# Performance work log

Hardware: AMD Instinct MI355X
Metric: run time of the kernel (lower is better)

Reference implementation:

```python
import jax, jax.numpy as jnp
import numpy as np

PAD, SOS, EOS = 0, 1, 2
NEG = -10000.0


def _lstm(x, w_ih, w_hh, b, reverse):
    # x: [T,B,E]; torch gate order i,f,g,o; b = b_ih + b_hh combined
    T, B, _ = x.shape
    H = w_hh.shape[1]
    xg = jnp.einsum('tbe,ge->tbg', x, w_ih) + b  # precompute input gates [T,B,4H]

    def step(carry, g):
        h, c = carry
        g = g + h @ w_hh.T
        i, f, gg, o = jnp.split(g, 4, axis=-1)
        c = jax.nn.sigmoid(f) * c + jax.nn.sigmoid(i) * jnp.tanh(gg)
        h = jax.nn.sigmoid(o) * jnp.tanh(c)
        return (h, c), h

    init = (jnp.zeros((B, H), x.dtype), jnp.zeros((B, H), x.dtype))
    _, hs = jax.lax.scan(step, init, xg, reverse=reverse)
    return hs  # [T,B,H]


def setup_inputs() -> dict:
    key = jax.random.key(0)
    T, B, V, E, H, K = 256, 64, 50000, 512, 512, 24
    ks = jax.random.split(key, 12)
    xw = jax.random.randint(ks[0], (T, B), 4, V)
    y_tags = jax.random.randint(ks[1], (T, B), 3, K)  # real tags, > EOS so mask is all ones
    y0 = jnp.concatenate([jnp.full((1, B), SOS, dtype=y_tags.dtype), y_tags], axis=0)  # [T+1,B]
    s = lambda k, sh: (jax.random.normal(k, sh, jnp.float32) * 0.02)
    emb = s(ks[2], (V, E))
    w_ih_f = s(ks[3], (4 * H, E)); w_hh_f = s(ks[4], (4 * H, H)); b_f = jnp.zeros((4 * H,), jnp.float32)
    w_ih_b = s(ks[5], (4 * H, E)); w_hh_b = s(ks[6], (4 * H, H)); b_b = jnp.zeros((4 * H,), jnp.float32)
    w_out = s(ks[7], (K, 2 * H)); b_out = jnp.zeros((K,), jnp.float32)
    trans = jax.random.normal(ks[8], (K, K), jnp.float32)
    trans = trans.at[SOS, :].set(NEG).at[:, EOS].set(NEG).at[:, PAD].set(NEG).at[PAD, :].set(NEG)
    trans = trans.at[PAD, EOS].set(0.0).at[PAD, PAD].set(0.0)
    return dict(xw=xw, y0=y0, emb=emb, w_ih_f=w_ih_f, w_hh_f=w_hh_f, b_f=b_f,
                w_ih_b=w_ih_b, w_hh_b=w_hh_b, b_b=b_b, w_out=w_out, b_out=b_out, trans=trans)


def reference(xw, y0, emb, w_ih_f, w_hh_f, b_f, w_ih_b, w_hh_b, b_b, w_out, b_out, trans):
    mask = (y0[1:] > PAD).astype(emb.dtype)  # [T,B]
    x = emb[xw]  # [T,B,E]
    hf = _lstm(x, w_ih_f, w_hh_f, b_f, reverse=False)
    hb = _lstm(x, w_ih_b, w_hh_b, b_b, reverse=True)
    h = jnp.concatenate([hf, hb], axis=-1) @ w_out.T + b_out  # [T,B,K]
    h = h * mask[:, :, None]
    B, K = h.shape[1], h.shape[2]

    # --- CRF partition function (forward algorithm) ---
    score0 = jnp.full((B, K), NEG, h.dtype).at[:, SOS].set(0.0)

    def step(score, inp):
        ht, mt = inp  # ht: [B,K], mt: [B]
        # new[b,j] = logsumexp_i(score[b,i] + ht[b,j] + trans[j,i])
        new = jax.nn.logsumexp(score[:, None, :] + ht[:, :, None] + trans[None, :, :], axis=2)
        return new * mt[:, None] + score * (1.0 - mt[:, None]), None

    score, _ = jax.lax.scan(step, score0, (h, mask))
    Z = jax.nn.logsumexp(score + trans[EOS], axis=1)  # [B]

    # --- gold path score ---
    emit = jnp.take_along_axis(h, y0[1:][:, :, None], axis=2)[..., 0]  # [T,B]
    tr = trans[y0[1:], y0[:-1]]  # [T,B]
    lens = mask.sum(0).astype(jnp.int32)  # [B]
    last = jnp.take_along_axis(y0, lens[None, :], axis=0)[0]  # y0[lens[b], b]
    gold = ((emit + tr) * mask).sum(0) + trans[EOS, last]  # [B]

    return jnp.mean(Z - gold)
```

## Files before the change

kernel.cpp:

```cpp
#include <hip/hip_runtime.h>

typedef __attribute__((ext_vector_type(8))) short short8;
typedef __attribute__((ext_vector_type(4))) float f32x4;

#define NEGV -10000.0f

__device__ __forceinline__ float bfu2f(unsigned short u) {
  unsigned int x = ((unsigned int)u) << 16;
  return __builtin_bit_cast(float, x);
}
__device__ __forceinline__ unsigned short f2bfu(float f) {
  unsigned int x = __builtin_bit_cast(unsigned int, f);
  x += 0x7fffu + ((x >> 16) & 1u);
  return (unsigned short)(x >> 16);
}
__device__ __forceinline__ float fsig(float x) {
  return 1.0f / (1.0f + __expf(-x));
}
__device__ __forceinline__ float ftanh(float x) {
  x = fminf(15.0f, fmaxf(-15.0f, x));
  float e = __expf(-2.0f * x);
  return (1.0f - e) / (1.0f + e);
}

__global__ __launch_bounds__(256) void prep_kernel(
    const float* __restrict__ wihf, const float* __restrict__ wihb,
    const float* __restrict__ whhf, const float* __restrict__ whhb,
    const float* __restrict__ wo, const float* __restrict__ bfv,
    const float* __restrict__ bbv,
    unsigned short* __restrict__ wih_c, unsigned short* __restrict__ whh_c,
    unsigned short* __restrict__ wout_c, float* __restrict__ bias_c) {
  size_t i = (size_t)blockIdx.x * 256 + threadIdx.x;
  const size_t n_half = 2048u * 512u;
  const size_t n_wih = 2u * n_half;
  const size_t n_wo = 24u * 1024u;
  if (i < n_wih) {
    float v = (i < n_half) ? wihf[i] : wihb[i - n_half];
    wih_c[i] = f2bfu(v);
  } else if (i < 2u * n_wih) {
    size_t j = i - n_wih;
    float v = (j < n_half) ? whhf[j] : whhb[j - n_half];
    whh_c[j] = f2bfu(v);
  } else if (i < 2u * n_wih + n_wo) {
    size_t j = i - 2u * n_wih;
    wout_c[j] = f2bfu(wo[j]);
  } else if (i < 2u * n_wih + n_wo + 4096u) {
    size_t j = i - 2u * n_wih - n_wo;
    bias_c[j] = (j < 2048u) ? bfv[j] : bbv[j - 2048u];
  }
}

__global__ __launch_bounds__(64) void gather_kernel(
    const int* __restrict__ xw, const float* __restrict__ emb,
    unsigned short* __restrict__ xbf) {
  int tb = blockIdx.x;
  int l = threadIdx.x;
  int tok = xw[tb];
  const float* src = emb + (size_t)tok * 512 + l * 8;
  short8 o;
#pragma unroll
  for (int j = 0; j < 8; ++j) o[j] = (short)f2bfu(src[j]);
  *(short8*)(xbf + (size_t)tb * 512 + l * 8) = o;
}

__global__ __launch_bounds__(256) void gemm_xg_kernel(
    const unsigned short* __restrict__ A,
    const unsigned short* __restrict__ Bm,
    const float* __restrict__ bias,
    unsigned short* __restrict__ C) {
  __shared__ alignas(16) char As[16384];
  __shared__ alignas(16) char Bs[16384];
  int m0 = blockIdx.x * 128, n0 = blockIdx.y * 128;
  int tid = threadIdx.x;
  int wv = tid >> 6, l = tid & 63;
  int wm = wv >> 1, wn = wv & 1;
  int col = l & 15, quad = l >> 4;
  f32x4 zero4 = {0.f, 0.f, 0.f, 0.f};
  f32x4 acc[4][4];
#pragma unroll
  for (int i = 0; i < 4; ++i)
#pragma unroll
    for (int j = 0; j < 4; ++j) acc[i][j] = zero4;
  for (int kt = 0; kt < 8; ++kt) {
#pragma unroll
    for (int q = 0; q < 4; ++q) {
      int o = q * 4096 + tid * 16;
      int row = o >> 7;
      int cb = o & 127;
      int swz = cb ^ ((row & 7) << 4);
      short8 va = *(const short8*)(A + (size_t)(m0 + row) * 512 + kt * 64 + (cb >> 1));
      *(short8*)(As + row * 128 + swz) = va;
      short8 vb = *(const short8*)(Bm + (size_t)(n0 + row) * 512 + kt * 64 + (cb >> 1));
      *(short8*)(Bs + row * 128 + swz) = vb;
    }
    __syncthreads();
#pragma unroll
    for (int kk = 0; kk < 2; ++kk) {
      short8 af[4], bf8[4];
#pragma unroll
      for (int mi = 0; mi < 4; ++mi) {
        int r = wm * 64 + mi * 16 + col;
        int cb = kk * 64 + quad * 16;
        af[mi] = *(const short8*)(As + r * 128 + (cb ^ ((r & 7) << 4)));
      }
#pragma unroll
      for (int ni = 0; ni < 4; ++ni) {
        int r = wn * 64 + ni * 16 + col;
        int cb = kk * 64 + quad * 16;
        bf8[ni] = *(const short8*)(Bs + r * 128 + (cb ^ ((r & 7) << 4)));
      }
#pragma unroll
      for (int mi = 0; mi < 4; ++mi)
#pragma unroll
        for (int ni = 0; ni < 4; ++ni)
          acc[mi][ni] = __builtin_amdgcn_mfma_f32_16x16x32_bf16(af[mi], bf8[ni], acc[mi][ni], 0, 0, 0);
    }
    __syncthreads();
  }
#pragma unroll
  for (int ni = 0; ni < 4; ++ni) {
    int cg = n0 + wn * 64 + ni * 16 + col;
    float bv = bias[cg];
#pragma unroll
    for (int mi = 0; mi < 4; ++mi) {
#pragma unroll
      for (int r = 0; r < 4; ++r) {
        int rg = m0 + wm * 64 + mi * 16 + quad * 4 + r;
        C[(size_t)rg * 4096 + cg] = f2bfu(acc[mi][ni][r] + bv);
      }
    }
  }
}

__global__ __launch_bounds__(64, 1) void scan_kernel(
    const unsigned short* __restrict__ whh,
    const unsigned short* __restrict__ xg,
    unsigned short* __restrict__ hfp,
    unsigned short* __restrict__ hbp) {
  __shared__ alignas(16) unsigned short tbuf[128];
  int wid = blockIdx.x;
  int l = threadIdx.x;
  int dir = wid & 1;
  int g = (wid >> 1) & 63;
  int wv = (wid >> 7) & 3;
  int u0 = g * 8;
  int col = l & 15, quad = l >> 4;
  int b_row = wv * 16 + quad * 4;
  short8 bfr[2][16];
#pragma unroll
  for (int n = 0; n < 2; ++n) {
    int blk = n * 2 + (col >> 3);
    int gr = blk * 512 + u0 + (col & 7);
    const char* base = (const char*)(whh + ((size_t)dir * 2048 + gr) * 512 + quad * 8);
#pragma unroll
    for (int kk = 0; kk < 16; ++kk)
      asm volatile("global_load_dwordx4 %0, %1, off" : "=v"(bfr[n][kk]) : "v"(base + kk * 64));
  }
  asm volatile("s_waitcnt vmcnt(0)" ::: "memory");
  unsigned short* hseq = dir ? hbp : hfp;
  float cst[4] = {0.f, 0.f, 0.f, 0.f};
  f32x4 zero4 = {0.f, 0.f, 0.f, 0.f};
  for (int s = 0; s < 256; ++s) {
    int t = dir ? (255 - s) : s;
    float xgv[2][4];
#pragma unroll
    for (int n = 0; n < 2; ++n) {
      int gc = dir * 2048 + (n * 2 + (col >> 3)) * 512 + u0 + (col & 7);
#pragma unroll
      for (int r = 0; r < 4; ++r)
        xgv[n][r] = bfu2f(xg[((size_t)t * 64 + b_row + r) * 4096 + gc]);
    }
    f32x4 a0 = zero4, a1 = zero4;
    if (s > 0) {
      int tprev = dir ? (t + 1) : (t - 1);
      const char* pbase = (const char*)hseq + (size_t)tprev * 65536 + quad * 1024 +
                          (wv * 16 + col) * 16;
      short8 af[16];
      unsigned long long bal;
      do {
#pragma unroll
        for (int kk = 0; kk < 16; ++kk)
          asm volatile("global_load_dwordx4 %0, %1, off sc0 sc1" : "=v"(af[kk]) : "v"(pbase + kk * 4096));
        asm volatile("s_waitcnt vmcnt(0)" ::: "memory");
        unsigned int anystale = 0u;
#pragma unroll
        for (int kk = 0; kk < 16; ++kk)
          anystale |= (((unsigned short)af[kk][0]) == 0xFFFFu) ? 1u : 0u;
        bal = __ballot(anystale != 0u);
      } while (bal != 0ull);
      __builtin_amdgcn_sched_barrier(0);
#pragma unroll
      for (int kk = 0; kk < 16; ++kk) {
        a0 = __builtin_amdgcn_mfma_f32_16x16x32_bf16(af[kk], bfr[0][kk], a0, 0, 0, 0);
        a1 = __builtin_amdgcn_mfma_f32_16x16x32_bf16(af[kk], bfr[1][kk], a1, 0, 0, 0);
      }
    }
    {
      bool low = (col < 8);
#pragma unroll
      for (int r = 0; r < 4; ++r) {
        float g0 = a0[r] + xgv[0][r];
        float g1 = a1[r] + xgv[1][r];
        float p0 = __shfl_xor(g0, 8);
        float p1 = __shfl_xor(g1, 8);
        float iv = low ? g0 : p0;
        float fv = low ? p0 : g0;
        float gv = low ? g1 : p1;
        float ov = low ? p1 : g1;
        float cn = fsig(fv) * cst[r] + fsig(iv) * ftanh(gv);
        cst[r] = cn;
        float hv = fsig(ov) * ftanh(cn);
        if (low) tbuf[(quad * 4 + r) * 8 + (col & 7)] = f2bfu(hv);
      }
    }
    asm volatile("s_waitcnt lgkmcnt(0)" ::: "memory");
    if (l < 16) {
      short8 hrow = *(const short8*)(tbuf + l * 8);
      char* dst = (char*)hseq + (size_t)t * 65536 + g * 1024 + (wv * 16 + l) * 16;
      asm volatile("global_store_dwordx4 %0, %1, off sc0 sc1" :: "v"(dst), "v"(hrow) : "memory");
    }
  }
}

__global__ __launch_bounds__(256) void logits_kernel(
    const unsigned short* __restrict__ hfp, const unsigned short* __restrict__ hbp,
    const unsigned short* __restrict__ wout, const float* __restrict__ bout,
    const int* __restrict__ y0, float* __restrict__ lg) {
  int t = blockIdx.x, tid = threadIdx.x;
  int b = tid >> 2, ks = tid & 3;
  int ytag = y0[(t + 1) * 64 + b];
  float mk = (ytag > 0) ? 1.f : 0.f;
  float av[6] = {0.f, 0.f, 0.f, 0.f, 0.f, 0.f};
  const char* pf = (const char*)hfp + (size_t)t * 65536;
  const char* pb = (const char*)hbp + (size_t)t * 65536;
  for (int uc = 0; uc < 64; ++uc) {
    short8 hv = *(const short8*)(pf + uc * 1024 + b * 16);
#pragma unroll
    for (int kk = 0; kk < 6; ++kk) {
      int k = ks * 6 + kk;
      short8 wv = *(const short8*)(wout + (size_t)k * 1024 + uc * 8);
#pragma unroll
      for (int j = 0; j < 8; ++j)
        av[kk] += bfu2f((unsigned short)hv[j]) * bfu2f((unsigned short)wv[j]);
    }
  }
  for (int uc = 0; uc < 64; ++uc) {
    short8 hv = *(const short8*)(pb + uc * 1024 + b * 16);
#pragma unroll
    for (int kk = 0; kk < 6; ++kk) {
      int k = ks * 6 + kk;
      short8 wv = *(const short8*)(wout + (size_t)k * 1024 + 512 + uc * 8);
#pragma unroll
      for (int j = 0; j < 8; ++j)
        av[kk] += bfu2f((unsigned short)hv[j]) * bfu2f((unsigned short)wv[j]);
    }
  }
#pragma unroll
  for (int kk = 0; kk < 6; ++kk) {
    int k = ks * 6 + kk;
    lg[((size_t)t * 64 + b) * 32 + k] = mk * (av[kk] + bout[k]);
  }
}

__global__ __launch_bounds__(64) void crf_kernel(
    const float* __restrict__ lg, const int* __restrict__ y0,
    const float* __restrict__ trans, float* __restrict__ res) {
  int b = blockIdx.x, l = threadIdx.x;
  __shared__ float tl[600];
  __shared__ float sc[24];
  for (int i = l; i < 576; i += 64) tl[(i / 24) * 25 + (i % 24)] = trans[i];
  if (l < 24) sc[l] = (l == 1) ? 0.f : NEGV;
  __syncthreads();
  float gold = 0.f;
  int lens = 0;
  for (int t = l; t < 256; t += 64) {
    int y1 = y0[(t + 1) * 64 + b];
    int yp = y0[t * 64 + b];
    if (y1 > 0) {
      gold += lg[((size_t)t * 64 + b) * 32 + y1] + tl[y1 * 25 + yp];
      lens += 1;
    }
  }
#pragma unroll
  for (int off = 32; off > 0; off >>= 1) {
    gold += __shfl_down(gold, off);
    lens += __shfl_down(lens, off);
  }
  gold = __shfl(gold, 0);
  lens = __shfl(lens, 0);
  int last = y0[lens * 64 + b];
  gold += tl[2 * 25 + last];
  int lc = (l < 24) ? l : 23;
  float trow[24];
#pragma unroll
  for (int j = 0; j < 24; ++j) trow[j] = tl[lc * 25 + j];
  for (int t = 0; t < 256; ++t) {
    int y1 = y0[(t + 1) * 64 + b];
    if (y1 > 0) {
      float ns = 0.f;
      if (l < 24) {
        float ht = lg[((size_t)t * 64 + b) * 32 + l];
        float mx = -3.0e38f;
        float sj[24];
#pragma unroll
        for (int j = 0; j < 24; ++j) {
          sj[j] = sc[j] + trow[j];
          mx = fmaxf(mx, sj[j]);
        }
        float sm = 0.f;
#pragma unroll
        for (int j = 0; j < 24; ++j) sm += __expf(sj[j] - mx);
        ns = ht + mx + __logf(sm);
      }
      __syncthreads();
      if (l < 24) sc[l] = ns;
      __syncthreads();
    }
  }
  float v = (l < 24) ? sc[l] + tl[2 * 25 + l] : -3.0e38f;
  float mx = v;
#pragma unroll
  for (int off = 32; off > 0; off >>= 1) mx = fmaxf(mx, __shfl_xor(mx, off));
  float se = (l < 24) ? __expf(v - mx) : 0.f;
#pragma unroll
  for (int off = 32; off > 0; off >>= 1) se += __shfl_xor(se, off);
  float Z = mx + __logf(se);
  if (l == 0) res[b] = Z - gold;
}

__global__ __launch_bounds__(64) void reduce_kernel(const float* __restrict__ res,
                                                    float* __restrict__ out) {
  int l = threadIdx.x;
  float v = res[l];
#pragma unroll
  for (int off = 32; off > 0; off >>= 1) v += __shfl_down(v, off);
  if (l == 0) out[0] = v * (1.0f / 64.0f);
}

extern "C" void kernel_launch(void* const* d_in, const int* in_sizes, int n_in,
                              void* d_out, int out_size, void* d_ws, size_t ws_size,
                              hipStream_t stream) {
  (void)in_sizes; (void)n_in; (void)out_size; (void)ws_size;
  const int* xw = (const int*)d_in[0];
  const int* y0 = (const int*)d_in[1];
  const float* emb = (const float*)d_in[2];
  const float* wihf = (const float*)d_in[3];
  const float* whhf = (const float*)d_in[4];
  const float* bfv = (const float*)d_in[5];
  const float* wihb = (const float*)d_in[6];
  const float* whhb = (const float*)d_in[7];
  const float* bbv = (const float*)d_in[8];
  const float* wo = (const float*)d_in[9];
  const float* bo = (const float*)d_in[10];
  const float* tr = (const float*)d_in[11];
  char* ws = (char*)d_ws;
  unsigned short* xg = (unsigned short*)(ws + 0);
  unsigned short* xbf = (unsigned short*)(ws + 134217728);
  unsigned short* wih_c = (unsigned short*)(ws + 150994944);
  unsigned short* whh_c = (unsigned short*)(ws + 155189248);
  unsigned short* wout_c = (unsigned short*)(ws + 159383552);
  float* bias_c = (float*)(ws + 159432704);
  unsigned short* hfp = (unsigned short*)(ws + 159449088);
  unsigned short* hbp = (unsigned short*)(ws + 176226304);
  float* lg = (float*)(ws + 193003520);
  float* res = (float*)(ws + 195104768);

  hipMemsetAsync(hfp, 0xFF, 16777216, stream);
  hipMemsetAsync(hbp, 0xFF, 16777216, stream);
  prep_kernel<<<16496, 256, 0, stream>>>(wihf, wihb, whhf, whhb, wo, bfv, bbv,
                                         wih_c, whh_c, wout_c, bias_c);
  gather_kernel<<<16384, 64, 0, stream>>>(xw, emb, xbf);
  gemm_xg_kernel<<<dim3(128, 32), 256, 0, stream>>>(xbf, wih_c, bias_c, xg);
  scan_kernel<<<512, 64, 0, stream>>>(whh_c, xg, hfp, hbp);
  logits_kernel<<<256, 256, 0, stream>>>(hfp, hbp, wout_c, bo, y0, lg);
  crf_kernel<<<64, 64, 0, stream>>>(lg, y0, tr, res);
  reduce_kernel<<<1, 64, 0, stream>>>(res, (float*)d_out);
}
```

Baseline: 1.250 ms.

## Speed up LSTM scan polling with L2-scoped loads, xg prefetch, and block remap

```diff
diff --git a/kernel.cpp b/kernel.cpp
--- a/kernel.cpp
+++ b/kernel.cpp
@@ -140,9 +140,10 @@
   __shared__ alignas(16) unsigned short tbuf[128];
   int wid = blockIdx.x;
   int l = threadIdx.x;
-  int dir = wid & 1;
-  int g = (wid >> 1) & 63;
-  int wv = (wid >> 7) & 3;
+  int c = wid & 7;
+  int dir = c & 1;
+  int wv = (c >> 1) & 3;
+  int g = wid >> 3;
   int u0 = g * 8;
   int col = l & 15, quad = l >> 4;
   int b_row = wv * 16 + quad * 4;
@@ -156,70 +157,110 @@
     for (int kk = 0; kk < 16; ++kk)
       asm volatile("global_load_dwordx4 %0, %1, off" : "=v"(bfr[n][kk]) : "v"(base + kk * 64));
   }
-  asm volatile("s_waitcnt vmcnt(0)" ::: "memory");
   unsigned short* hseq = dir ? hbp : hfp;
+  int gc0 = dir * 2048 + (col >> 3) * 512 + u0 + (col & 7);
   float cst[4] = {0.f, 0.f, 0.f, 0.f};
   f32x4 zero4 = {0.f, 0.f, 0.f, 0.f};
-  for (int s = 0; s < 256; ++s) {
-    int t = dir ? (255 - s) : s;
-    float xgv[2][4];
-#pragma unroll
-    for (int n = 0; n < 2; ++n) {
-      int gc = dir * 2048 + (n * 2 + (col >> 3)) * 512 + u0 + (col & 7);
-#pragma unroll
-      for (int r = 0; r < 4; ++r)
-        xgv[n][r] = bfu2f(xg[((size_t)t * 64 + b_row + r) * 4096 + gc]);
-    }
-    f32x4 a0 = zero4, a1 = zero4;
-    if (s > 0) {
-      int tprev = dir ? (t + 1) : (t - 1);
-      const char* pbase = (const char*)hseq + (size_t)tprev * 65536 + quad * 1024 +
-                          (wv * 16 + col) * 16;
-      short8 af[16];
-      unsigned long long bal;
-      do {
-#pragma unroll
-        for (int kk = 0; kk < 16; ++kk)
-          asm volatile("global_load_dwordx4 %0, %1, off sc0 sc1" : "=v"(af[kk]) : "v"(pbase + kk * 4096));
-        asm volatile("s_waitcnt vmcnt(0)" ::: "memory");
-        unsigned int anystale = 0u;
-#pragma unroll
-        for (int kk = 0; kk < 16; ++kk)
-          anystale |= (((unsigned short)af[kk][0]) == 0xFFFFu) ? 1u : 0u;
-        bal = __ballot(anystale != 0u);
-      } while (bal != 0ull);
-      __builtin_amdgcn_sched_barrier(0);
-#pragma unroll
-      for (int kk = 0; kk < 16; ++kk) {
-        a0 = __builtin_amdgcn_mfma_f32_16x16x32_bf16(af[kk], bfr[0][kk], a0, 0, 0, 0);
-        a1 = __builtin_amdgcn_mfma_f32_16x16x32_bf16(af[kk], bfr[1][kk], a1, 0, 0, 0);
-      }
-    }
-    {
-      bool low = (col < 8);
-#pragma unroll
-      for (int r = 0; r < 4; ++r) {
-        float g0 = a0[r] + xgv[0][r];
-        float g1 = a1[r] + xgv[1][r];
-        float p0 = __shfl_xor(g0, 8);
-        float p1 = __shfl_xor(g1, 8);
-        float iv = low ? g0 : p0;
-        float fv = low ? p0 : g0;
-        float gv = low ? g1 : p1;
-        float ov = low ? p1 : g1;
-        float cn = fsig(fv) * cst[r] + fsig(iv) * ftanh(gv);
-        cst[r] = cn;
-        float hv = fsig(ov) * ftanh(cn);
-        if (low) tbuf[(quad * 4 + r) * 8 + (col & 7)] = f2bfu(hv);
-      }
-    }
-    asm volatile("s_waitcnt lgkmcnt(0)" ::: "memory");
-    if (l < 16) {
-      short8 hrow = *(const short8*)(tbuf + l * 8);
-      char* dst = (char*)hseq + (size_t)t * 65536 + g * 1024 + (wv * 16 + l) * 16;
-      asm volatile("global_store_dwordx4 %0, %1, off sc0 sc1" :: "v"(dst), "v"(hrow) : "memory");
-    }
-  }
+  short8 af[16];
+  int usefast = 1;
+  unsigned int xA[8], xB[8];
+  {
+    int t0 = dir ? 255 : 0;
+#pragma unroll
+    for (int r = 0; r < 4; ++r) {
+      const char* xa = (const char*)(xg + ((size_t)t0 * 64 + b_row + r) * 4096 + gc0);
+      asm volatile("global_load_ushort %0, %1, off" : "=v"(xA[r]) : "v"(xa));
+      asm volatile("global_load_ushort %0, %1, off" : "=v"(xA[4 + r]) : "v"(xa + 2048));
+    }
+  }
+  asm volatile("s_waitcnt vmcnt(0)" ::: "memory");
+  __builtin_amdgcn_sched_barrier(0);
+
+#define SCAN_STEP(S_, XU_, XP_)                                                             \
+  {                                                                                         \
+    int s_ = (S_);                                                                          \
+    int t_ = dir ? (255 - s_) : s_;                                                         \
+    f32x4 a0 = zero4, a1 = zero4;                                                           \
+    if (s_ > 0) {                                                                           \
+      int tprev = t_ + (dir ? 1 : -1);                                                      \
+      const char* pbase = (const char*)hseq + (size_t)tprev * 65536 + quad * 1024 +         \
+                          (wv * 16 + col) * 16;                                             \
+      unsigned long long bal = 1ull;                                                        \
+      if (usefast) {                                                                        \
+        for (int tryi = 0; tryi < 8 && bal != 0ull; ++tryi) {                               \
+          _Pragma("unroll") for (int kk = 0; kk < 16; ++kk)                                 \
+              asm volatile("global_load_dwordx4 %0, %1, off sc0"                            \
+                           : "=v"(af[kk]) : "v"(pbase + kk * 4096));                        \
+          asm volatile("s_waitcnt vmcnt(0)" ::: "memory");                                  \
+          __builtin_amdgcn_sched_barrier(0);                                                \
+          unsigned int st_ = 0u;                                                            \
+          _Pragma("unroll") for (int kk = 0; kk < 16; ++kk)                                 \
+              st_ |= (((unsigned short)af[kk][0]) == 0xFFFFu) ? 1u : 0u;                    \
+          bal = __ballot(st_ != 0u);                                                        \
+        }                                                                                   \
+        if (bal != 0ull) usefast = 0;                                                       \
+      }                                                                                     \
+      while (bal != 0ull) {                                                                 \
+        _Pragma("unroll") for (int kk = 0; kk < 16; ++kk)                                   \
+            asm volatile("global_load_dwordx4 %0, %1, off sc0 sc1"                          \
+                         : "=v"(af[kk]) : "v"(pbase + kk * 4096));                          \
+        asm volatile("s_waitcnt vmcnt(0)" ::: "memory");                                    \
+        __builtin_amdgcn_sched_barrier(0);                                                  \
+        unsigned int st_ = 0u;                                                              \
+        _Pragma("unroll") for (int kk = 0; kk < 16; ++kk)                                   \
+            st_ |= (((unsigned short)af[kk][0]) == 0xFFFFu) ? 1u : 0u;                      \
+        bal = __ballot(st_ != 0u);                                                          \
+      }                                                                                     \
+      __builtin_amdgcn_s_setprio(1);                                                        \
+      __builtin_amdgcn_sched_barrier(0);                                                    \
+      _Pragma("unroll") for (int kk = 0; kk < 16; ++kk) {                                   \
+        a0 = __builtin_amdgcn_mfma_f32_16x16x32_bf16(af[kk], bfr[0][kk], a0, 0, 0, 0);      \
+        a1 = __builtin_amdgcn_mfma_f32_16x16x32_bf16(af[kk], bfr[1][kk], a1, 0, 0, 0);      \
+      }                                                                                     \
+    }                                                                                       \
+    {                                                                                       \
+      int sn = (s_ < 255) ? (s_ + 1) : 255;                                                 \
+      int tn = dir ? (255 - sn) : sn;                                                       \
+      _Pragma("unroll") for (int r = 0; r < 4; ++r) {                                       \
+        const char* xa = (const char*)(xg + ((size_t)tn * 64 + b_row + r) * 4096 + gc0);    \
+        asm volatile("global_load_ushort %0, %1, off" : "=v"(XP_[r]) : "v"(xa));            \
+        asm volatile("global_load_ushort %0, %1, off" : "=v"(XP_[4 + r]) : "v"(xa + 2048)); \
+      }                                                                                     \
+    }                                                                                       \
+    {                                                                                       \
+      bool low = (col < 8);                                                                 \
+      _Pragma("unroll") for (int r = 0; r < 4; ++r) {                                       \
+        float g0 = a0[r] + bfu2f((unsigned short)XU_[r]);                                   \
+        float g1 = a1[r] + bfu2f((unsigned short)XU_[4 + r]);                               \
+        float p0 = __shfl_xor(g0, 8);                                                       \
+        float p1 = __shfl_xor(g1, 8);                                                       \
+        float iv = low ? g0 : p0;                                                           \
+        float fv = low ? p0 : g0;                                                           \
+        float gv = low ? g1 : p1;                                                           \
+        float ov = low ? p1 : g1;                                                           \
+        float cn = fsig(fv) * cst[r] + fsig(iv) * ftanh(gv);                                \
+        cst[r] = cn;                                                                        \
+        float hv = fsig(ov) * ftanh(cn);                                                    \
+        if (low) tbuf[(quad * 4 + r) * 8 + (col & 7)] = f2bfu(hv);                          \
+      }                                                                                     \
+    }                                                                                       \
+    asm volatile("s_waitcnt lgkmcnt(0)" ::: "memory");                                      \
+    if (l < 16) {                                                                           \
+      short8 hrow = *(const short8*)(tbuf + l * 8);                                         \
+      char* dst = (char*)hseq + (size_t)t_ * 65536 + g * 1024 + (wv * 16 + l) * 16;         \
+      asm volatile("global_store_dwordx4 %0, %1, off sc0 sc1" ::"v"(dst), "v"(hrow)         \
+                   : "memory");                                                             \
+      asm volatile("global_store_dwordx4 %0, %1, off sc0" ::"v"(dst), "v"(hrow)             \
+                   : "memory");                                                             \
+    }                                                                                       \
+    __builtin_amdgcn_s_setprio(0);                                                          \
+  }
+
+  for (int it = 0; it < 128; ++it) {
+    SCAN_STEP(2 * it, xA, xB);
+    SCAN_STEP(2 * it + 1, xB, xA);
+  }
+#undef SCAN_STEP
 }
 
 __global__ __launch_bounds__(256) void logits_kernel(
```

After: 1.208 ms. 1.04x faster.

## Fuse embedding gather, input-gate GEMM and LSTM scan into one persistent kernel

Applied to the files above, without the earlier changes.

```diff
diff --git a/kernel.cpp b/kernel.cpp
--- a/kernel.cpp
+++ b/kernel.cpp
@@ -50,174 +50,203 @@
   }
 }
 
-__global__ __launch_bounds__(64) void gather_kernel(
-    const int* __restrict__ xw, const float* __restrict__ emb,
-    unsigned short* __restrict__ xbf) {
-  int tb = blockIdx.x;
-  int l = threadIdx.x;
-  int tok = xw[tb];
-  const float* src = emb + (size_t)tok * 512 + l * 8;
-  short8 o;
-#pragma unroll
-  for (int j = 0; j < 8; ++j) o[j] = (short)f2bfu(src[j]);
-  *(short8*)(xbf + (size_t)tb * 512 + l * 8) = o;
-}
-
-__global__ __launch_bounds__(256) void gemm_xg_kernel(
-    const unsigned short* __restrict__ A,
-    const unsigned short* __restrict__ Bm,
+__global__ __launch_bounds__(256, 1) void fused_kernel(
+    const int* __restrict__ xw,
+    const float* __restrict__ emb,
+    const unsigned short* __restrict__ wih,
     const float* __restrict__ bias,
-    unsigned short* __restrict__ C) {
+    const unsigned short* __restrict__ whh,
+    unsigned short* __restrict__ xg,
+    unsigned short* __restrict__ hfp,
+    unsigned short* __restrict__ hbp) {
   __shared__ alignas(16) char As[16384];
   __shared__ alignas(16) char Bs[16384];
-  int m0 = blockIdx.x * 128, n0 = blockIdx.y * 128;
-  int tid = threadIdx.x;
-  int wv = tid >> 6, l = tid & 63;
-  int wm = wv >> 1, wn = wv & 1;
-  int col = l & 15, quad = l >> 4;
-  f32x4 zero4 = {0.f, 0.f, 0.f, 0.f};
-  f32x4 acc[4][4];
-#pragma unroll
-  for (int i = 0; i < 4; ++i)
-#pragma unroll
-    for (int j = 0; j < 4; ++j) acc[i][j] = zero4;
-  for (int kt = 0; kt < 8; ++kt) {
-#pragma unroll
-    for (int q = 0; q < 4; ++q) {
-      int o = q * 4096 + tid * 16;
-      int row = o >> 7;
-      int cb = o & 127;
-      int swz = cb ^ ((row & 7) << 4);
-      short8 va = *(const short8*)(A + (size_t)(m0 + row) * 512 + kt * 64 + (cb >> 1));
-      *(short8*)(As + row * 128 + swz) = va;
-      short8 vb = *(const short8*)(Bm + (size_t)(n0 + row) * 512 + kt * 64 + (cb >> 1));
-      *(short8*)(Bs + row * 128 + swz) = vb;
-    }
-    __syncthreads();
-#pragma unroll
-    for (int kk = 0; kk < 2; ++kk) {
-      short8 af[4], bf8[4];
+  int gid = blockIdx.x;
+  if (gid < 4096) {
+    int bx = gid >> 5, by = gid & 31;
+    int m_eff = (bx & 1) ? (127 - (bx >> 1)) : (bx >> 1);
+    int m0 = m_eff * 128, n0 = by * 128;
+    int tid = threadIdx.x;
+    int wv = tid >> 6, l = tid & 63;
+    int wm = wv >> 1, wn = wv & 1;
+    int col = l & 15, quad = l >> 4;
+    int tok[4];
+#pragma unroll
+    for (int q = 0; q < 4; ++q) tok[q] = xw[m0 + ((q * 4096 + tid * 16) >> 7)];
+    f32x4 zero4 = {0.f, 0.f, 0.f, 0.f};
+    f32x4 acc[4][4];
+#pragma unroll
+    for (int i = 0; i < 4; ++i)
+#pragma unroll
+      for (int j = 0; j < 4; ++j) acc[i][j] = zero4;
+    for (int kt = 0; kt < 8; ++kt) {
+#pragma unroll
+      for (int q = 0; q < 4; ++q) {
+        int o = q * 4096 + tid * 16;
+        int row = o >> 7;
+        int cb = o & 127;
+        int swz = cb ^ ((row & 7) << 4);
+        const float* sa = emb + (size_t)tok[q] * 512 + kt * 64 + (cb >> 1);
+        f32x4 f0 = *(const f32x4*)sa;
+        f32x4 f1 = *(const f32x4*)(sa + 4);
+        short8 va;
+#pragma unroll
+        for (int j = 0; j < 4; ++j) {
+          va[j] = (short)f2bfu(f0[j]);
+          va[4 + j] = (short)f2bfu(f1[j]);
+        }
+        *(short8*)(As + row * 128 + swz) = va;
+        short8 vb = *(const short8*)(wih + (size_t)(n0 + row) * 512 + kt * 64 + (cb >> 1));
+        *(short8*)(Bs + row * 128 + swz) = vb;
+      }
+      __syncthreads();
+#pragma unroll
+      for (int kk = 0; kk < 2; ++kk) {
+        short8 af[4], bf8[4];
+#pragma unroll
+        for (int mi = 0; mi < 4; ++mi) {
+          int r = wm * 64 + mi * 16 + col;
+          int cb = kk * 64 + quad * 16;
+          af[mi] = *(const short8*)(As + r * 128 + (cb ^ ((r & 7) << 4)));
+        }
+#pragma unroll
+        for (int ni = 0; ni < 4; ++ni) {
+          int r = wn * 64 + ni * 16 + col;
+          int cb = kk * 64 + quad * 16;
+          bf8[ni] = *(const short8*)(Bs + r * 128 + (cb ^ ((r & 7) << 4)));
+        }
+#pragma unroll
+        for (int mi = 0; mi < 4; ++mi)
+#pragma unroll
+          for (int ni = 0; ni < 4; ++ni)
+            acc[mi][ni] = __builtin_amdgcn_mfma_f32_16x16x32_bf16(af[mi], bf8[ni], acc[mi][ni], 0, 0, 0);
+      }
+      __syncthreads();
+    }
+#pragma unroll
+    for (int ni = 0; ni < 4; ++ni) {
+      int cg = n0 + wn * 64 + ni * 16 + col;
+      float bv = bias[cg];
 #pragma unroll
       for (int mi = 0; mi < 4; ++mi) {
-        int r = wm * 64 + mi * 16 + col;
-        int cb = kk * 64 + quad * 16;
-        af[mi] = *(const short8*)(As + r * 128 + (cb ^ ((r & 7) << 4)));
-      }
-#pragma unroll
-      for (int ni = 0; ni < 4; ++ni) {
-        int r = wn * 64 + ni * 16 + col;
-        int cb = kk * 64 + quad * 16;
-        bf8[ni] = *(const short8*)(Bs + r * 128 + (cb ^ ((r & 7) << 4)));
-      }
-#pragma unroll
-      for (int mi = 0; mi < 4; ++mi)
-#pragma unroll
-        for (int ni = 0; ni < 4; ++ni)
-          acc[mi][ni] = __builtin_amdgcn_mfma_f32_16x16x32_bf16(af[mi], bf8[ni], acc[mi][ni], 0, 0, 0);
-    }
-    __syncthreads();
-  }
-#pragma unroll
-  for (int ni = 0; ni < 4; ++ni) {
-    int cg = n0 + wn * 64 + ni * 16 + col;
-    float bv = bias[cg];
-#pragma unroll
-    for (int mi = 0; mi < 4; ++mi) {
+#pragma unroll
+        for (int r = 0; r < 4; ++r) {
+          int rg = m0 + wm * 64 + mi * 16 + quad * 4 + r;
+          unsigned int cv = f2bfu(acc[mi][ni][r] + bv);
+          unsigned short* cp = xg + (size_t)rg * 4096 + cg;
+          asm volatile("global_store_short %0, %1, off sc0 sc1" ::"v"(cp), "v"(cv) : "memory");
+        }
+      }
+    }
+  } else {
+    if (threadIdx.x >= 64) return;
+    int wid = gid - 4096;
+    int l = threadIdx.x;
+    int dir = wid & 1;
+    int g = (wid >> 1) & 63;
+    int wv = (wid >> 7) & 3;
+    int u0 = g * 8;
+    int col = l & 15, quad = l >> 4;
+    int b_row = wv * 16 + quad * 4;
+    unsigned short* tbuf = (unsigned short*)As;
+    short8 bfr[2][16];
+#pragma unroll
+    for (int n = 0; n < 2; ++n) {
+      int blk = n * 2 + (col >> 3);
+      int gr = blk * 512 + u0 + (col & 7);
+      const char* base = (const char*)(whh + ((size_t)dir * 2048 + gr) * 512 + quad * 8);
+#pragma unroll
+      for (int kk = 0; kk < 16; ++kk)
+        asm volatile("global_load_dwordx4 %0, %1, off" : "=v"(bfr[n][kk]) : "v"(base + kk * 64));
+    }
+    asm volatile("s_waitcnt vmcnt(0)" ::: "memory");
+    unsigned short* hseq = dir ? hbp : hfp;
+    int gc0 = dir * 2048 + (col >> 3) * 512 + u0 + (col & 7);
+    float cst[4] = {0.f, 0.f, 0.f, 0.f};
+    f32x4 zero4 = {0.f, 0.f, 0.f, 0.f};
+    short8 af[16];
+    unsigned int xv[8];
+    for (int s = 0; s < 256; ++s) {
+      int t_ = dir ? (255 - s) : s;
 #pragma unroll
       for (int r = 0; r < 4; ++r) {
-        int rg = m0 + wm * 64 + mi * 16 + quad * 4 + r;
-        C[(size_t)rg * 4096 + cg] = f2bfu(acc[mi][ni][r] + bv);
-      }
-    }
-  }
-}
-
-__global__ __launch_bounds__(64, 1) void scan_kernel(
-    const unsigned short* __restrict__ whh,
-    const unsigned short* __restrict__ xg,
-    unsigned short* __restrict__ hfp,
-    unsigned short* __restrict__ hbp) {
-  __shared__ alignas(16) unsigned short tbuf[128];
-  int wid = blockIdx.x;
-  int l = threadIdx.x;
-  int dir = wid & 1;
-  int g = (wid >> 1) & 63;
-  int wv = (wid >> 7) & 3;
-  int u0 = g * 8;
-  int col = l & 15, quad = l >> 4;
-  int b_row = wv * 16 + quad * 4;
-  short8 bfr[2][16];
-#pragma unroll
-  for (int n = 0; n < 2; ++n) {
-    int blk = n * 2 + (col >> 3);
-    int gr = blk * 512 + u0 + (col & 7);
-    const char* base = (const char*)(whh + ((size_t)dir * 2048 + gr) * 512 + quad * 8);
-#pragma unroll
-    for (int kk = 0; kk < 16; ++kk)
-      asm volatile("global_load_dwordx4 %0, %1, off" : "=v"(bfr[n][kk]) : "v"(base + kk * 64));
-  }
-  asm volatile("s_waitcnt vmcnt(0)" ::: "memory");
-  unsigned short* hseq = dir ? hbp : hfp;
-  float cst[4] = {0.f, 0.f, 0.f, 0.f};
-  f32x4 zero4 = {0.f, 0.f, 0.f, 0.f};
-  for (int s = 0; s < 256; ++s) {
-    int t = dir ? (255 - s) : s;
-    float xgv[2][4];
-#pragma unroll
-    for (int n = 0; n < 2; ++n) {
-      int gc = dir * 2048 + (n * 2 + (col >> 3)) * 512 + u0 + (col & 7);
-#pragma unroll
-      for (int r = 0; r < 4; ++r)
-        xgv[n][r] = bfu2f(xg[((size_t)t * 64 + b_row + r) * 4096 + gc]);
-    }
-    f32x4 a0 = zero4, a1 = zero4;
-    if (s > 0) {
-      int tprev = dir ? (t + 1) : (t - 1);
-      const char* pbase = (const char*)hseq + (size_t)tprev * 65536 + quad * 1024 +
-                          (wv * 16 + col) * 16;
-      short8 af[16];
-      unsigned long long bal;
-      do {
-#pragma unroll
-        for (int kk = 0; kk < 16; ++kk)
-          asm volatile("global_load_dwordx4 %0, %1, off sc0 sc1" : "=v"(af[kk]) : "v"(pbase + kk * 4096));
+        const char* xa = (const char*)(xg + ((size_t)t_ * 64 + b_row + r) * 4096 + gc0);
+        asm volatile("global_load_ushort %0, %1, off sc0 sc1" : "=v"(xv[r]) : "v"(xa));
+        asm volatile("global_load_ushort %0, %1, off sc0 sc1" : "=v"(xv[4 + r]) : "v"(xa + 2048));
+      }
+      f32x4 a0 = zero4, a1 = zero4;
+      if (s > 0) {
+        int tprev = t_ + (dir ? 1 : -1);
+        const char* pbase = (const char*)hseq + (size_t)tprev * 65536 + quad * 1024 +
+                            (wv * 16 + col) * 16;
+        unsigned long long bal;
+        do {
+#pragma unroll
+          for (int kk = 0; kk < 16; ++kk)
+            asm volatile("global_load_dwordx4 %0, %1, off sc0 sc1" : "=v"(af[kk]) : "v"(pbase + kk * 4096));
+          asm volatile("s_waitcnt vmcnt(0)" ::: "memory");
+          __builtin_amdgcn_sched_barrier(0);
+          unsigned int st = 0u;
+#pragma unroll
+          for (int kk = 0; kk < 16; ++kk)
+            st |= (((unsigned short)af[kk][0]) == 0xFFFFu) ? 1u : 0u;
+          bal = __ballot(st != 0u);
+        } while (bal != 0ull);
+      } else {
         asm volatile("s_waitcnt vmcnt(0)" ::: "memory");
-        unsigned int anystale = 0u;
-#pragma unroll
-        for (int kk = 0; kk < 16; ++kk)
-          anystale |= (((unsigned short)af[kk][0]) == 0xFFFFu) ? 1u : 0u;
-        bal = __ballot(anystale != 0u);
-      } while (bal != 0ull);
-      __builtin_amdgcn_sched_barrier(0);
-#pragma unroll
-      for (int kk = 0; kk < 16; ++kk) {
-        a0 = __builtin_amdgcn_mfma_f32_16x16x32_bf16(af[kk], bfr[0][kk], a0, 0, 0, 0);
-        a1 = __builtin_amdgcn_mfma_f32_16x16x32_bf16(af[kk], bfr[1][kk], a1, 0, 0, 0);
-      }
-    }
-    {
-      bool low = (col < 8);
-#pragma unroll
-      for (int r = 0; r < 4; ++r) {
-        float g0 = a0[r] + xgv[0][r];
-        float g1 = a1[r] + xgv[1][r];
-        float p0 = __shfl_xor(g0, 8);
-        float p1 = __shfl_xor(g1, 8);
-        float iv = low ? g0 : p0;
-        float fv = low ? p0 : g0;
-        float gv = low ? g1 : p1;
-        float ov = low ? p1 : g1;
-        float cn = fsig(fv) * cst[r] + fsig(iv) * ftanh(gv);
-        cst[r] = cn;
-        float hv = fsig(ov) * ftanh(cn);
-        if (low) tbuf[(quad * 4 + r) * 8 + (col & 7)] = f2bfu(hv);
-      }
-    }
-    asm volatile("s_waitcnt lgkmcnt(0)" ::: "memory");
-    if (l < 16) {
-      short8 hrow = *(const short8*)(tbuf + l * 8);
-      char* dst = (char*)hseq + (size_t)t * 65536 + g * 1024 + (wv * 16 + l) * 16;
-      asm volatile("global_store_dwordx4 %0, %1, off sc0 sc1" :: "v"(dst), "v"(hrow) : "memory");
+        __builtin_amdgcn_sched_barrier(0);
+      }
+      {
+        unsigned int stx = 0u;
+#pragma unroll
+        for (int r = 0; r < 8; ++r) stx |= (xv[r] == 0xFFFFu) ? 1u : 0u;
+        unsigned long long balx = __ballot(stx != 0u);
+        while (balx != 0ull) {
+#pragma unroll
+          for (int r = 0; r < 4; ++r) {
+            const char* xa = (const char*)(xg + ((size_t)t_ * 64 + b_row + r) * 4096 + gc0);
+            asm volatile("global_load_ushort %0, %1, off sc0 sc1" : "=v"(xv[r]) : "v"(xa));
+            asm volatile("global_load_ushort %0, %1, off sc0 sc1" : "=v"(xv[4 + r]) : "v"(xa + 2048));
+          }
+          asm volatile("s_waitcnt vmcnt(0)" ::: "memory");
+          __builtin_amdgcn_sched_barrier(0);
+          stx = 0u;
+#pragma unroll
+          for (int r = 0; r < 8; ++r) stx |= (xv[r] == 0xFFFFu) ? 1u : 0u;
+          balx = __ballot(stx != 0u);
+        }
+      }
+      if (s > 0) {
+#pragma unroll
+        for (int kk = 0; kk < 16; ++kk) {
+          a0 = __builtin_amdgcn_mfma_f32_16x16x32_bf16(af[kk], bfr[0][kk], a0, 0, 0, 0);
+          a1 = __builtin_amdgcn_mfma_f32_16x16x32_bf16(af[kk], bfr[1][kk], a1, 0, 0, 0);
+        }
+      }
+      {
+        bool low = (col < 8);
+#pragma unroll
+        for (int r = 0; r < 4; ++r) {
+          float g0 = a0[r] + bfu2f((unsigned short)xv[r]);
+          float g1 = a1[r] + bfu2f((unsigned short)xv[4 + r]);
+          float p0 = __shfl_xor(g0, 8);
+          float p1 = __shfl_xor(g1, 8);
+          float iv = low ? g0 : p0;
+          float fv = low ? p0 : g0;
+          float gv = low ? g1 : p1;
+          float ov = low ? p1 : g1;
+          float cn = fsig(fv) * cst[r] + fsig(iv) * ftanh(gv);
+          cst[r] = cn;
+          float hv = fsig(ov) * ftanh(cn);
+          if (low) tbuf[(quad * 4 + r) * 8 + (col & 7)] = f2bfu(hv);
+        }
+      }
+      asm volatile("s_waitcnt lgkmcnt(0)" ::: "memory");
+      if (l < 16) {
+        short8 hrow = *(const short8*)(tbuf + l * 8);
+        char* dst = (char*)hseq + (size_t)t_ * 65536 + g * 1024 + (wv * 16 + l) * 16;
+        asm volatile("global_store_dwordx4 %0, %1, off sc0 sc1" ::"v"(dst), "v"(hrow) : "memory");
+      }
     }
   }
 }
@@ -355,7 +384,6 @@
   const float* tr = (const float*)d_in[11];
   char* ws = (char*)d_ws;
   unsigned short* xg = (unsigned short*)(ws + 0);
-  unsigned short* xbf = (unsigned short*)(ws + 134217728);
   unsigned short* wih_c = (unsigned short*)(ws + 150994944);
   unsigned short* whh_c = (unsigned short*)(ws + 155189248);
   unsigned short* wout_c = (unsigned short*)(ws + 159383552);
@@ -365,13 +393,12 @@
   float* lg = (float*)(ws + 193003520);
   float* res = (float*)(ws + 195104768);
 
+  hipMemsetAsync(xg, 0xFF, 134217728, stream);
   hipMemsetAsync(hfp, 0xFF, 16777216, stream);
   hipMemsetAsync(hbp, 0xFF, 16777216, stream);
   prep_kernel<<<16496, 256, 0, stream>>>(wihf, wihb, whhf, whhb, wo, bfv, bbv,
                                          wih_c, whh_c, wout_c, bias_c);
-  gather_kernel<<<16384, 64, 0, stream>>>(xw, emb, xbf);
-  gemm_xg_kernel<<<dim3(128, 32), 256, 0, stream>>>(xbf, wih_c, bias_c, xg);
-  scan_kernel<<<512, 64, 0, stream>>>(whh_c, xg, hfp, hbp);
+  fused_kernel<<<4608, 256, 0, stream>>>(xw, emb, wih_c, bias_c, whh_c, xg, hfp, hbp);
   logits_kernel<<<256, 256, 0, stream>>>(hfp, hbp, wout_c, bo, y0, lg);
   crf_kernel<<<64, 64, 0, stream>>>(lg, y0, tr, res);
   reduce_kernel<<<1, 64, 0, stream>>>(res, (float*)d_out);
```

After: 1.769 ms. 1.41x slower.

## Fuse embedding gather into input GEMM and use MFMA for logits

Applied to the files above, without the earlier changes.

```diff
diff --git a/kernel.cpp b/kernel.cpp
--- a/kernel.cpp
+++ b/kernel.cpp
@@ -50,21 +50,9 @@
   }
 }
 
-__global__ __launch_bounds__(64) void gather_kernel(
-    const int* __restrict__ xw, const float* __restrict__ emb,
-    unsigned short* __restrict__ xbf) {
-  int tb = blockIdx.x;
-  int l = threadIdx.x;
-  int tok = xw[tb];
-  const float* src = emb + (size_t)tok * 512 + l * 8;
-  short8 o;
-#pragma unroll
-  for (int j = 0; j < 8; ++j) o[j] = (short)f2bfu(src[j]);
-  *(short8*)(xbf + (size_t)tb * 512 + l * 8) = o;
-}
-
 __global__ __launch_bounds__(256) void gemm_xg_kernel(
-    const unsigned short* __restrict__ A,
+    const int* __restrict__ xw,
+    const float* __restrict__ emb,
     const unsigned short* __restrict__ Bm,
     const float* __restrict__ bias,
     unsigned short* __restrict__ C) {
@@ -75,6 +63,9 @@
   int wv = tid >> 6, l = tid & 63;
   int wm = wv >> 1, wn = wv & 1;
   int col = l & 15, quad = l >> 4;
+  int tok[4];
+#pragma unroll
+  for (int q = 0; q < 4; ++q) tok[q] = xw[m0 + ((q * 4096 + tid * 16) >> 7)];
   f32x4 zero4 = {0.f, 0.f, 0.f, 0.f};
   f32x4 acc[4][4];
 #pragma unroll
@@ -88,7 +79,15 @@
       int row = o >> 7;
       int cb = o & 127;
       int swz = cb ^ ((row & 7) << 4);
-      short8 va = *(const short8*)(A + (size_t)(m0 + row) * 512 + kt * 64 + (cb >> 1));
+      const float* sa = emb + (size_t)tok[q] * 512 + kt * 64 + (cb >> 1);
+      f32x4 f0 = *(const f32x4*)sa;
+      f32x4 f1 = *(const f32x4*)(sa + 4);
+      short8 va;
+#pragma unroll
+      for (int j = 0; j < 4; ++j) {
+        va[j] = (short)f2bfu(f0[j]);
+        va[4 + j] = (short)f2bfu(f1[j]);
+      }
       *(short8*)(As + row * 128 + swz) = va;
       short8 vb = *(const short8*)(Bm + (size_t)(n0 + row) * 512 + kt * 64 + (cb >> 1));
       *(short8*)(Bs + row * 128 + swz) = vb;
@@ -226,39 +225,43 @@
     const unsigned short* __restrict__ hfp, const unsigned short* __restrict__ hbp,
     const unsigned short* __restrict__ wout, const float* __restrict__ bout,
     const int* __restrict__ y0, float* __restrict__ lg) {
-  int t = blockIdx.x, tid = threadIdx.x;
-  int b = tid >> 2, ks = tid & 3;
-  int ytag = y0[(t + 1) * 64 + b];
-  float mk = (ytag > 0) ? 1.f : 0.f;
-  float av[6] = {0.f, 0.f, 0.f, 0.f, 0.f, 0.f};
+  int t = blockIdx.x;
+  int w = threadIdx.x >> 6, l = threadIdx.x & 63;
+  int nt = w & 1, mh = w >> 1;
+  int col = l & 15, quad = l >> 4;
+  int wr = nt * 16 + col;
+  if (wr > 23) wr = 23;
+  short8 bw[32];
+#pragma unroll
+  for (int kk = 0; kk < 32; ++kk)
+    bw[kk] = *(const short8*)(wout + (size_t)wr * 1024 + kk * 32 + quad * 8);
+  f32x4 zero4 = {0.f, 0.f, 0.f, 0.f};
   const char* pf = (const char*)hfp + (size_t)t * 65536;
   const char* pb = (const char*)hbp + (size_t)t * 65536;
-  for (int uc = 0; uc < 64; ++uc) {
-    short8 hv = *(const short8*)(pf + uc * 1024 + b * 16);
-#pragma unroll
-    for (int kk = 0; kk < 6; ++kk) {
-      int k = ks * 6 + kk;
-      short8 wv = *(const short8*)(wout + (size_t)k * 1024 + uc * 8);
-#pragma unroll
-      for (int j = 0; j < 8; ++j)
-        av[kk] += bfu2f((unsigned short)hv[j]) * bfu2f((unsigned short)wv[j]);
-    }
-  }
-  for (int uc = 0; uc < 64; ++uc) {
-    short8 hv = *(const short8*)(pb + uc * 1024 + b * 16);
-#pragma unroll
-    for (int kk = 0; kk < 6; ++kk) {
-      int k = ks * 6 + kk;
-      short8 wv = *(const short8*)(wout + (size_t)k * 1024 + 512 + uc * 8);
-#pragma unroll
-      for (int j = 0; j < 8; ++j)
-        av[kk] += bfu2f((unsigned short)hv[j]) * bfu2f((unsigned short)wv[j]);
-    }
-  }
-#pragma unroll
-  for (int kk = 0; kk < 6; ++kk) {
-    int k = ks * 6 + kk;
-    lg[((size_t)t * 64 + b) * 32 + k] = mk * (av[kk] + bout[k]);
+#pragma unroll
+  for (int mt = 0; mt < 2; ++mt) {
+    int b0 = mh * 32 + mt * 16;
+    f32x4 acc = zero4;
+#pragma unroll
+    for (int kk = 0; kk < 16; ++kk) {
+      short8 a = *(const short8*)(pf + (kk * 4 + quad) * 1024 + (b0 + col) * 16);
+      acc = __builtin_amdgcn_mfma_f32_16x16x32_bf16(a, bw[kk], acc, 0, 0, 0);
+    }
+#pragma unroll
+    for (int kk = 0; kk < 16; ++kk) {
+      short8 a = *(const short8*)(pb + (kk * 4 + quad) * 1024 + (b0 + col) * 16);
+      acc = __builtin_amdgcn_mfma_f32_16x16x32_bf16(a, bw[16 + kk], acc, 0, 0, 0);
+    }
+    int ko = nt * 16 + col;
+    if (ko < 24) {
+      float bv = bout[ko];
+#pragma unroll
+      for (int r = 0; r < 4; ++r) {
+        int b = b0 + quad * 4 + r;
+        float mk = (y0[(t + 1) * 64 + b] > 0) ? 1.f : 0.f;
+        lg[((size_t)t * 64 + b) * 32 + ko] = mk * (acc[r] + bv);
+      }
+    }
   }
 }
 
@@ -355,7 +358,6 @@
   const float* tr = (const float*)d_in[11];
   char* ws = (char*)d_ws;
   unsigned short* xg = (unsigned short*)(ws + 0);
-  unsigned short* xbf = (unsigned short*)(ws + 134217728);
   unsigned short* wih_c = (unsigned short*)(ws + 150994944);
   unsigned short* whh_c = (unsigned short*)(ws + 155189248);
   unsigned short* wout_c = (unsigned short*)(ws + 159383552);
@@ -369,8 +371,7 @@
   hipMemsetAsync(hbp, 0xFF, 16777216, stream);
   prep_kernel<<<16496, 256, 0, stream>>>(wihf, wihb, whhf, whhb, wo, bfv, bbv,
                                          wih_c, whh_c, wout_c, bias_c);
-  gather_kernel<<<16384, 64, 0, stream>>>(xw, emb, xbf);
-  gemm_xg_kernel<<<dim3(128, 32), 256, 0, stream>>>(xbf, wih_c, bias_c, xg);
+  gemm_xg_kernel<<<dim3(128, 32), 256, 0, stream>>>(xw, emb, wih_c, bias_c, xg);
   scan_kernel<<<512, 64, 0, stream>>>(whh_c, xg, hfp, hbp);
   logits_kernel<<<256, 256, 0, stream>>>(hfp, hbp, wout_c, bo, y0, lg);
   crf_kernel<<<64, 64, 0, stream>>>(lg, y0, tr, res);
```

Measured after the change: 1.183 ms. 1.06x faster.
